# Optimization experiments

Hardware: AMD Instinct MI355X
Metric: run time of the kernel (lower is better)

## Reference

```python
import jax, jax.numpy as jnp
import numpy as np

NX, NY, NZ = 512, 512, 1
C_BEV = 128
C_BEFORE = C_BEV // NZ  # features per z-slice
B = 4
P_PER_BATCH = 80000


def setup_inputs() -> dict:
    key = jax.random.key(0)
    P = B * P_PER_BATCH
    pillar_features = jax.random.normal(key, (P, C_BEFORE), dtype=jnp.float32)
    # Build coords with unique spatial cells per batch so scatter order is irrelevant.
    rng = np.random.default_rng(0)
    cells = NZ * NY * NX
    coords_np = np.empty((P, 4), dtype=np.int32)
    for b in range(B):  # loop over tiny fixed batch count, setup only
        flat = rng.choice(cells, size=P_PER_BATCH, replace=False)
        z = flat // (NY * NX)
        y = (flat // NX) % NY
        x = flat % NX
        s = slice(b * P_PER_BATCH, (b + 1) * P_PER_BATCH)
        coords_np[s, 0] = b
        coords_np[s, 1] = z
        coords_np[s, 2] = y
        coords_np[s, 3] = x
    return {
        "batch_size": B,
        "pillar_features": pillar_features,
        "coords": jnp.asarray(coords_np),
    }


def reference(batch_size, pillar_features, coords):
    # Fused single-pass scatter: global flat index = b*(nz*ny*nx) + z*ny*nx + y*nx + x
    cells = NZ * NY * NX
    flat = (coords[:, 0].astype(jnp.int32) * cells
            + coords[:, 1].astype(jnp.int32) * (NY * NX)
            + coords[:, 2].astype(jnp.int32) * NX
            + coords[:, 3].astype(jnp.int32))
    canvas = jnp.zeros((batch_size * cells, C_BEFORE), dtype=pillar_features.dtype)
    canvas = canvas.at[flat].set(pillar_features)
    # [B*nz*ny*nx, C] -> [B, nz, ny, nx, C] -> [B, C, nz, ny, nx] -> [B, C*nz, ny, nx]
    canvas = canvas.reshape(batch_size, NZ, NY, NX, C_BEFORE)
    canvas = jnp.transpose(canvas, (0, 4, 1, 2, 3))
    return canvas.reshape(batch_size, C_BEFORE * NZ, NY, NX)
```

## Files before the change

kernel.cpp:

```cpp
#include <hip/hip_runtime.h>


#define NXD 512
#define NYD 512
#define NZD 1
#define CB  128
#define CELLS (NXD * NYD * NZD)

#define TILE 128
#define NTHR 512

typedef float f4 __attribute__((ext_vector_type(4)));

__global__ void k_scatter_idx(const int* __restrict__ coords,
                              int* __restrict__ map, int P) {
    int p = blockIdx.x * blockDim.x + threadIdx.x;
    if (p >= P) return;
    int4 c = ((const int4*)coords)[p];
    int cell = c.y * (NYD * NXD) + c.z * NXD + c.w;
    map[c.x * CELLS + cell] = p;
}

__global__ __launch_bounds__(NTHR) void k_gather(const float* __restrict__ feat,
                                                 const int* __restrict__ map,
                                                 float* __restrict__ out) {
    __shared__ int pidx[TILE];
    __shared__ f4  ldsC[CB][TILE / 4];

    const int t = threadIdx.x;
    const int tiles_per_b = CELLS / TILE;
    const int b = blockIdx.x / tiles_per_b;
    const int cell_base = (blockIdx.x % tiles_per_b) * TILE;

    if (t < TILE) pidx[t] = map[b * CELLS + cell_base + t];
    __syncthreads();

    {
        const int c4 = t & 31;
        const int r0 = t >> 5;
        int idxr[8];
        #pragma unroll
        for (int rr = 0; rr < 8; ++rr) idxr[rr] = pidx[rr * 16 + r0];
        #pragma unroll
        for (int rr = 0; rr < 8; ++rr) {
            const int x = rr * 16 + r0;
            f4 v = (f4)(0.f);
            if (idxr[rr] >= 0)
                v = ((const f4*)feat)[(size_t)idxr[rr] * (CB / 4) + c4];
            const int slot = (x >> 2) ^ (c4 & 7);
            const int xe   = x & 3;
            ((float*)&ldsC[c4 * 4 + 0][slot])[xe] = v.x;
            ((float*)&ldsC[c4 * 4 + 1][slot])[xe] = v.y;
            ((float*)&ldsC[c4 * 4 + 2][slot])[xe] = v.z;
            ((float*)&ldsC[c4 * 4 + 3][slot])[xe] = v.w;
        }
    }
    __syncthreads();

    {
        const int x4 = t & 31;
        const int cr = t >> 5;
        float* outb = out + (size_t)b * CB * CELLS + cell_base;
        #pragma unroll
        for (int cc = 0; cc < 8; ++cc) {
            const int c = cc * 16 + cr;
            f4 v = ldsC[c][x4 ^ ((c >> 2) & 7)];
            *reinterpret_cast<f4*>(outb + (size_t)c * CELLS + x4 * 4) = v;
        }
    }
}

extern "C" void kernel_launch(void* const* d_in, const int* in_sizes, int n_in,
                              void* d_out, int out_size, void* d_ws, size_t ws_size,
                              hipStream_t stream) {
    const float* feat   = (const float*)d_in[1];
    const int*   coords = (const int*)d_in[2];
    float*       out    = (float*)d_out;
    int*         map    = (int*)d_ws;

    const int B = out_size / (CB * CELLS);
    const int P = in_sizes[1] / CB;
    const int n_map = B * CELLS;

    (void)hipMemsetAsync(map, 0xFF, (size_t)n_map * sizeof(int), stream);
    k_scatter_idx<<<(P + 255) / 256, 256, 0, stream>>>(coords, map, P);
    k_gather<<<B * (CELLS / TILE), NTHR, 0, stream>>>(feat, map, out);
}
```

Measured before the change: 191.1 us.

## Retile gather over 512-cell spans split into four channel groups

Each block of the gather kernel now covers 512 cells and 32 of the 128 channels, with four channel-group blocks per span, instead of 128 cells and all channels. Stores now form contiguous 2KB rows per channel, which should make output writes longer and more coalesced, and the XOR swizzle in shared memory is dropped. In exchange, each feature row is read as four separate 128-byte chunks by different blocks, the map is read four times, and the unswizzled shared-memory writes may hit bank conflicts.

```diff
diff --git a/kernel.cpp b/kernel.cpp
--- a/kernel.cpp
+++ b/kernel.cpp
@@ -7,7 +7,9 @@
 #define CB  128
 #define CELLS (NXD * NYD * NZD)
 
-#define TILE 128
+#define SPAN 512
+#define CGS  4
+#define CGW  32
 #define NTHR 512
 
 typedef float f4 __attribute__((ext_vector_type(4)));
@@ -24,48 +26,48 @@
 __global__ __launch_bounds__(NTHR) void k_gather(const float* __restrict__ feat,
                                                  const int* __restrict__ map,
                                                  float* __restrict__ out) {
-    __shared__ int pidx[TILE];
-    __shared__ f4  ldsC[CB][TILE / 4];
+    __shared__ int   pidx[SPAN];
+    __shared__ float ldsT[CGW][SPAN];
 
-    const int t = threadIdx.x;
-    const int tiles_per_b = CELLS / TILE;
-    const int b = blockIdx.x / tiles_per_b;
-    const int cell_base = (blockIdx.x % tiles_per_b) * TILE;
+    const int t    = threadIdx.x;
+    const int cg   = blockIdx.x & (CGS - 1);
+    const int rest = blockIdx.x >> 2;
+    const int span = rest & (CELLS / SPAN - 1);
+    const int b    = rest >> 9;
+    const int cell_base = span * SPAN;
 
-    if (t < TILE) pidx[t] = map[b * CELLS + cell_base + t];
+    pidx[t] = map[b * CELLS + cell_base + t];
     __syncthreads();
 
     {
-        const int c4 = t & 31;
-        const int r0 = t >> 5;
+        const int q  = t & 7;
+        const int xc = t >> 3;
         int idxr[8];
         #pragma unroll
-        for (int rr = 0; rr < 8; ++rr) idxr[rr] = pidx[rr * 16 + r0];
+        for (int p = 0; p < 8; ++p) idxr[p] = pidx[p * 64 + xc];
         #pragma unroll
-        for (int rr = 0; rr < 8; ++rr) {
-            const int x = rr * 16 + r0;
+        for (int p = 0; p < 8; ++p) {
+            const int x = p * 64 + xc;
             f4 v = (f4)(0.f);
-            if (idxr[rr] >= 0)
-                v = ((const f4*)feat)[(size_t)idxr[rr] * (CB / 4) + c4];
-            const int slot = (x >> 2) ^ (c4 & 7);
-            const int xe   = x & 3;
-            ((float*)&ldsC[c4 * 4 + 0][slot])[xe] = v.x;
-            ((float*)&ldsC[c4 * 4 + 1][slot])[xe] = v.y;
-            ((float*)&ldsC[c4 * 4 + 2][slot])[xe] = v.z;
-            ((float*)&ldsC[c4 * 4 + 3][slot])[xe] = v.w;
+            if (idxr[p] >= 0)
+                v = ((const f4*)feat)[(size_t)idxr[p] * (CB / 4) + cg * 8 + q];
+            ldsT[q * 4 + 0][x] = v.x;
+            ldsT[q * 4 + 1][x] = v.y;
+            ldsT[q * 4 + 2][x] = v.z;
+            ldsT[q * 4 + 3][x] = v.w;
         }
     }
     __syncthreads();
 
     {
-        const int x4 = t & 31;
-        const int cr = t >> 5;
+        const int x4 = t & 127;
+        const int c0 = t >> 7;
         float* outb = out + (size_t)b * CB * CELLS + cell_base;
         #pragma unroll
-        for (int cc = 0; cc < 8; ++cc) {
-            const int c = cc * 16 + cr;
-            f4 v = ldsC[c][x4 ^ ((c >> 2) & 7)];
-            *reinterpret_cast<f4*>(outb + (size_t)c * CELLS + x4 * 4) = v;
+        for (int p = 0; p < 8; ++p) {
+            const int c = p * 4 + c0;
+            f4 v = *(const f4*)&ldsT[c][x4 * 4];
+            *(f4*)(outb + (size_t)(cg * CGW + c) * CELLS + x4 * 4) = v;
         }
     }
 }
@@ -84,5 +86,5 @@
 
     (void)hipMemsetAsync(map, 0xFF, (size_t)n_map * sizeof(int), stream);
     k_scatter_idx<<<(P + 255) / 256, 256, 0, stream>>>(coords, map, P);
-    k_gather<<<B * (CELLS / TILE), NTHR, 0, stream>>>(feat, map, out);
+    k_gather<<<B * (CELLS / SPAN) * CGS, NTHR, 0, stream>>>(feat, map, out);
 }
```

Measured after the change: 222.1 us. 1.16x slower.

## Restructure gather as persistent per-wave 16-cell tiles without block barriers

Applied to the files above, without the earlier changes.

The gather kernel now launches a fixed grid of 2048 blocks. Each of the four waves in a block loops over independent 16-cell tiles, so the block no longer works on one 128-cell tile. Map indices are shared within the wave by shuffle instead of through LDS plus __syncthreads, and each wave transposes through its own padded LDS region. This removes block-level barriers and lets waves overlap their loads and stores. In exchange each output row write is only 64 contiguous bytes per channel, where it used to be 512, which may hurt write coalescing.

```diff
diff --git a/kernel.cpp b/kernel.cpp
--- a/kernel.cpp
+++ b/kernel.cpp
@@ -7,8 +7,8 @@
 #define CB  128
 #define CELLS (NXD * NYD * NZD)
 
-#define TILE 128
-#define NTHR 512
+#define TPW  16
+#define NTHR 256
 
 typedef float f4 __attribute__((ext_vector_type(4)));
 
@@ -23,49 +23,49 @@
 
 __global__ __launch_bounds__(NTHR) void k_gather(const float* __restrict__ feat,
                                                  const int* __restrict__ map,
-                                                 float* __restrict__ out) {
-    __shared__ int pidx[TILE];
-    __shared__ f4  ldsC[CB][TILE / 4];
+                                                 float* __restrict__ out,
+                                                 int ntiles) {
+    __shared__ f4 lds4[4][TPW * 33];
 
-    const int t = threadIdx.x;
-    const int tiles_per_b = CELLS / TILE;
-    const int b = blockIdx.x / tiles_per_b;
-    const int cell_base = (blockIdx.x % tiles_per_b) * TILE;
+    const int lane = threadIdx.x & 63;
+    const int w    = threadIdx.x >> 6;
+    f4* __restrict__ L = lds4[w];
+    const float* __restrict__ Lf = (const float*)L;
 
-    if (t < TILE) pidx[t] = map[b * CELLS + cell_base + t];
-    __syncthreads();
+    const int gw     = blockIdx.x * 4 + w;
+    const int nwaves = gridDim.x * 4;
 
-    {
-        const int c4 = t & 31;
-        const int r0 = t >> 5;
-        int idxr[8];
-        #pragma unroll
-        for (int rr = 0; rr < 8; ++rr) idxr[rr] = pidx[rr * 16 + r0];
+    const int hi  = lane >> 5;
+    const int c4  = lane & 31;
+    const int ch0 = lane >> 2;
+    const int x4  = lane & 3;
+
+    for (int tile = gw; tile < ntiles; tile += nwaves) {
+        const int b         = tile / (CELLS / TPW);
+        const int cell_base = (tile % (CELLS / TPW)) * TPW;
+
+        int idx0 = -1;
+        if (lane < TPW) idx0 = map[b * CELLS + cell_base + lane];
+
         #pragma unroll
         for (int rr = 0; rr < 8; ++rr) {
-            const int x = rr * 16 + r0;
+            const int row = rr * 2 + hi;
+            const int idx = __shfl(idx0, row);
             f4 v = (f4)(0.f);
-            if (idxr[rr] >= 0)
-                v = ((const f4*)feat)[(size_t)idxr[rr] * (CB / 4) + c4];
-            const int slot = (x >> 2) ^ (c4 & 7);
-            const int xe   = x & 3;
-            ((float*)&ldsC[c4 * 4 + 0][slot])[xe] = v.x;
-            ((float*)&ldsC[c4 * 4 + 1][slot])[xe] = v.y;
-            ((float*)&ldsC[c4 * 4 + 2][slot])[xe] = v.z;
-            ((float*)&ldsC[c4 * 4 + 3][slot])[xe] = v.w;
+            if (idx >= 0) v = ((const f4*)feat)[(size_t)idx * (CB / 4) + c4];
+            L[row * 33 + c4] = v;
         }
-    }
-    __syncthreads();
 
-    {
-        const int x4 = t & 31;
-        const int cr = t >> 5;
-        float* outb = out + (size_t)b * CB * CELLS + cell_base;
+        float* outb = out + (size_t)b * CB * CELLS + cell_base + x4 * 4;
         #pragma unroll
         for (int cc = 0; cc < 8; ++cc) {
-            const int c = cc * 16 + cr;
-            f4 v = ldsC[c][x4 ^ ((c >> 2) & 7)];
-            *reinterpret_cast<f4*>(outb + (size_t)c * CELLS + x4 * 4) = v;
+            const int c = cc * 16 + ch0;
+            f4 v;
+            v.x = Lf[(x4 * 4 + 0) * 132 + c];
+            v.y = Lf[(x4 * 4 + 1) * 132 + c];
+            v.z = Lf[(x4 * 4 + 2) * 132 + c];
+            v.w = Lf[(x4 * 4 + 3) * 132 + c];
+            *(f4*)(outb + (size_t)c * CELLS) = v;
         }
     }
 }
@@ -80,9 +80,10 @@
 
     const int B = out_size / (CB * CELLS);
     const int P = in_sizes[1] / CB;
-    const int n_map = B * CELLS;
+    const int n_map  = B * CELLS;
+    const int ntiles = B * (CELLS / TPW);
 
     (void)hipMemsetAsync(map, 0xFF, (size_t)n_map * sizeof(int), stream);
     k_scatter_idx<<<(P + 255) / 256, 256, 0, stream>>>(coords, map, P);
-    k_gather<<<B * (CELLS / TILE), NTHR, 0, stream>>>(feat, map, out);
+    k_gather<<<2048, NTHR, 0, stream>>>(feat, map, out, ntiles);
 }
```

Result: slower. 287.8 us (+50.6%).
